# Kernel optimization log

Hardware: AMD Instinct MI355X
Metric: run time of the kernel (lower is better)

## Reference

```python
import jax, jax.numpy as jnp
import numpy as np

N_NODES = 100000
N_EDGES = 3200000
NUM_FEATURES = 128


def gcn_conv(x, edge_index, W, b):
    """PyG-style GCNConv: symmetric normalization with self-loops.
    x: [N, F_in], edge_index: [2, E] (row=src, col=dst), W: [F_in, F_out], b: [F_out].
    """
    n = x.shape[0]
    h = x @ W  # [N, F_out]
    # add self loops
    loop = jnp.arange(n, dtype=edge_index.dtype)
    row = jnp.concatenate([edge_index[0], loop])  # src
    col = jnp.concatenate([edge_index[1], loop])  # dst
    # degree of destination nodes (with self loops), edge weight = 1
    ones = jnp.ones(row.shape[0], dtype=h.dtype)
    deg = jax.ops.segment_sum(ones, col, num_segments=n)  # [N]
    dinv = jnp.where(deg > 0, jax.lax.rsqrt(deg), 0.0)
    norm = dinv[row] * dinv[col]  # [E+N]
    msg = h[row] * norm[:, None]  # gather + scale, [E+N, F_out]
    out = jax.ops.segment_sum(msg, col, num_segments=n)  # scatter-add
    return out + b


def setup_inputs() -> dict:
    key = jax.random.key(0)
    k1, k2, k3, k4 = jax.random.split(key, 4)
    x = jax.random.normal(k1, (N_NODES, NUM_FEATURES), dtype=jnp.float32)
    edge_index = jax.random.randint(k2, (2, N_EDGES), 0, N_NODES, dtype=jnp.int64)
    W1 = jax.random.normal(k3, (NUM_FEATURES, 16), dtype=jnp.float32) * (1.0 / np.sqrt(NUM_FEATURES))
    b1 = jnp.zeros((16,), dtype=jnp.float32)
    W2 = jax.random.normal(k4, (16, 2), dtype=jnp.float32) * (1.0 / np.sqrt(16.0))
    b2 = jnp.zeros((2,), dtype=jnp.float32)
    return {"x": x, "edge_index": edge_index, "W1": W1, "b1": b1, "W2": W2, "b2": b2}


def reference(x, edge_index, W1, b1, W2, b2):
    h = gcn_conv(x, edge_index, W1, b1)
    h = jax.nn.relu(h)
    out = gcn_conv(h, edge_index, W2, b2)
    return out
```

## Files before the change

### kernel.cpp

```cpp
#include <hip/hip_runtime.h>

#define N_FEAT 128
#define F1 16
#define F2 2
#define XPAD 132
#define NPB 512
#define NPB_SHIFT 9
#define BMAX 256
#define CHUNK 8192

typedef int   ev_i4 __attribute__((ext_vector_type(4)));
typedef float ev_f4 __attribute__((ext_vector_type(4)));

__device__ __forceinline__ int4 nt_load_i4(const void* p) {
    ev_i4 v = __builtin_nontemporal_load((const ev_i4*)p);
    return make_int4(v.x, v.y, v.z, v.w);
}
__device__ __forceinline__ int nt_load_i(const int* p) {
    return __builtin_nontemporal_load(p);
}
__device__ __forceinline__ float4 nt_load_f4(const void* p) {
    ev_f4 v = __builtin_nontemporal_load((const ev_f4*)p);
    return make_float4(v.x, v.y, v.z, v.w);
}

__global__ __launch_bounds__(256) void bin_kernel(const int* __restrict__ rowi,
        const int* __restrict__ coli, int* __restrict__ gcur,
        int* __restrict__ ebin, int E, int cap) {
    __shared__ int stage[CHUNK];
    __shared__ unsigned char sbkt[CHUNK];
    __shared__ int cnt[BMAX];
    __shared__ int pos[BMAX];
    __shared__ int runb[BMAX];
    int t = threadIdx.x;
    int base = blockIdx.x * CHUNK;
    int nval = E - base; if (nval > CHUNK) nval = CHUNK;
    cnt[t] = 0;
    __syncthreads();

    int cbuf[32];
#pragma unroll
    for (int j = 0; j < 8; ++j) {
        int idx = base + ((j << 8) + t) * 4;
        if (idx + 3 < E) {
            int4 c4 = nt_load_i4(coli + idx);
            cbuf[j * 4 + 0] = c4.x; cbuf[j * 4 + 1] = c4.y;
            cbuf[j * 4 + 2] = c4.z; cbuf[j * 4 + 3] = c4.w;
        } else {
#pragma unroll
            for (int u = 0; u < 4; ++u) {
                int i2 = idx + u;
                cbuf[j * 4 + u] = (i2 < E) ? coli[i2] : -1;
            }
        }
    }
#pragma unroll
    for (int k = 0; k < 32; ++k)
        if (cbuf[k] >= 0) atomicAdd(&cnt[cbuf[k] >> NPB_SHIFT], 1);
    __syncthreads();

    pos[t] = cnt[t];
    __syncthreads();
    for (int off = 1; off < BMAX; off <<= 1) {
        int a = (t >= off) ? pos[t - off] : 0;
        __syncthreads();
        pos[t] += a;
        __syncthreads();
    }
    int myc = cnt[t];
    int excl = pos[t] - myc;
    if (myc > 0) {
        int g = atomicAdd(&gcur[t], myc);
        runb[t] = t * cap + g - excl;
    }
    __syncthreads();
    cnt[t] = excl;
    __syncthreads();

#pragma unroll
    for (int j = 0; j < 8; ++j) {
        int idx = base + ((j << 8) + t) * 4;
        int rr[4];
        if (idx + 3 < E) {
            int4 r4 = nt_load_i4(rowi + idx);
            rr[0] = r4.x; rr[1] = r4.y; rr[2] = r4.z; rr[3] = r4.w;
        } else {
#pragma unroll
            for (int u = 0; u < 4; ++u) {
                int i2 = idx + u;
                rr[u] = (i2 < E) ? rowi[i2] : 0;
            }
        }
#pragma unroll
        for (int u = 0; u < 4; ++u) {
            int c = cbuf[j * 4 + u];
            if (c >= 0) {
                int b = c >> NPB_SHIFT;
                int lp = atomicAdd(&cnt[b], 1);
                stage[lp] = (rr[u] << NPB_SHIFT) | (c & (NPB - 1));
                sbkt[lp] = (unsigned char)b;
            }
        }
    }
    __syncthreads();
    for (int i = t; i < nval; i += 256)
        ebin[runb[sbkt[i]] + i] = stage[i];
}

__global__ __launch_bounds__(1024) void csr_kernel(const int* __restrict__ gcur,
        const int* __restrict__ ebin, int* __restrict__ rstart, int* __restrict__ degA,
        float* __restrict__ dinv, int* __restrict__ csr, int N, int cap) {
    __shared__ int cnt[NPB];
    __shared__ int sd[NPB];
    int b = blockIdx.x, t = threadIdx.x;
    if (t < NPB) cnt[t] = 0;
    __syncthreads();
    int s = b * cap;
    int e = s + gcur[b];
    for (int i = s + t; i < e; i += 4096) {
        int w[4];
#pragma unroll
        for (int u = 0; u < 4; ++u) {
            int idx = i + u * 1024;
            w[u] = (idx < e) ? nt_load_i(&ebin[idx]) : -1;
        }
#pragma unroll
        for (int u = 0; u < 4; ++u)
            if (w[u] >= 0) atomicAdd(&cnt[w[u] & (NPB - 1)], 1);
    }
    __syncthreads();
    int d = (t < NPB) ? cnt[t] : 0;
    if (t < NPB) sd[t] = d;
    __syncthreads();
    for (int off = 1; off < NPB; off <<= 1) {
        int a = (t < NPB && t >= off) ? sd[t - off] : 0;
        __syncthreads();
        if (t < NPB) sd[t] += a;
        __syncthreads();
    }
    int rs = s + ((t < NPB) ? (sd[t] - d) : 0);
    if (t < NPB) {
        int g = (b << NPB_SHIFT) + t;
        if (g < N) {
            rstart[g] = rs;
            degA[g] = d;
            dinv[g] = rsqrtf((float)(d + 1));
        }
        cnt[t] = rs;
    }
    __syncthreads();
    for (int i = s + t; i < e; i += 4096) {
        int w[4];
#pragma unroll
        for (int u = 0; u < 4; ++u) {
            int idx = i + u * 1024;
            w[u] = (idx < e) ? nt_load_i(&ebin[idx]) : -1;
        }
#pragma unroll
        for (int u = 0; u < 4; ++u) {
            if (w[u] >= 0) {
                int p = atomicAdd(&cnt[w[u] & (NPB - 1)], 1);
                csr[p] = w[u] >> NPB_SHIFT;
            }
        }
    }
}

__global__ __launch_bounds__(256) void gemm1_kernel(
    const float* __restrict__ x, const float* __restrict__ W1,
    const float* __restrict__ dinv, float* __restrict__ hs, int N) {
    __shared__ __align__(16) float wsT[F1][XPAD];
    __shared__ __align__(16) float xs[16][XPAD];
    int t = threadIdx.x;
    for (int i = t; i < N_FEAT * F1; i += 256) {
        int k = i >> 4, f = i & 15;
        wsT[f][k] = W1[i];
    }
    int row0 = blockIdx.x * 16;
    for (int i = t; i < 16 * (N_FEAT / 4); i += 256) {
        int r = i >> 5, k4 = i & 31;
        int row = row0 + r;
        float4 v = (row < N) ? nt_load_f4(x + (size_t)row * N_FEAT + k4 * 4)
                             : make_float4(0.f, 0.f, 0.f, 0.f);
        *(float4*)&xs[r][k4 * 4] = v;
    }
    __syncthreads();
    int rr = t >> 4, f = t & 15;
    int row = row0 + rr;
    if (row >= N) return;
    float acc = 0.f;
#pragma unroll
    for (int k4 = 0; k4 < 32; ++k4) {
        float4 xv = *(const float4*)&xs[rr][k4 * 4];
        float4 wv = *(const float4*)&wsT[f][k4 * 4];
        acc += xv.x * wv.x + xv.y * wv.y + xv.z * wv.z + xv.w * wv.w;
    }
    hs[(size_t)row * F1 + f] = acc * dinv[row];
}

__global__ __launch_bounds__(256) void agg1_kernel(const int* __restrict__ rstart,
        const int* __restrict__ degA, const int* __restrict__ csr,
        const float* __restrict__ hs, const float* __restrict__ dinv,
        const float* __restrict__ b1, const float* __restrict__ W2,
        float* __restrict__ hs2, int N) {
    int t = threadIdx.x;
    int g = blockIdx.x * 16 + (t >> 4);
    int f = t & 15;
    if (g >= N) return;
    int s = rstart[g], e = s + degA[g];
    float acc = hs[(size_t)g * F1 + f];
    int k = s;
    for (; k + 4 <= e; k += 4) {
        int s0 = nt_load_i(&csr[k]);
        int s1 = nt_load_i(&csr[k + 1]);
        int s2 = nt_load_i(&csr[k + 2]);
        int s3 = nt_load_i(&csr[k + 3]);
        float v0 = hs[(size_t)s0 * F1 + f];
        float v1 = hs[(size_t)s1 * F1 + f];
        float v2 = hs[(size_t)s2 * F1 + f];
        float v3 = hs[(size_t)s3 * F1 + f];
        acc += (v0 + v1) + (v2 + v3);
    }
    for (; k < e; ++k) acc += hs[(size_t)nt_load_i(&csr[k]) * F1 + f];
    float di = dinv[g];
    float o = fmaxf(di * acc + b1[f], 0.f);
    float h0 = o * W2[f * F2 + 0];
    float h1 = o * W2[f * F2 + 1];
#pragma unroll
    for (int off = 1; off < 16; off <<= 1) {
        h0 += __shfl_xor(h0, off);
        h1 += __shfl_xor(h1, off);
    }
    if (f == 0) *(float2*)&hs2[(size_t)g * 2] = make_float2(di * h0, di * h1);
}

__global__ __launch_bounds__(256) void agg2_kernel(const int* __restrict__ rstart,
        const int* __restrict__ degA, const int* __restrict__ csr,
        const float* __restrict__ hs2, const float* __restrict__ dinv,
        const float* __restrict__ b2, float* __restrict__ out, int N) {
    int t = threadIdx.x;
    int g = blockIdx.x * 64 + (t >> 2);
    int l = t & 3;
    if (g >= N) return;
    int j = l & 1, c = l >> 1;
    int s = rstart[g], e = s + degA[g];
    float acc = 0.f;
    int k = s + c;
    for (; k + 6 < e; k += 8) {
        int s0 = nt_load_i(&csr[k]);
        int s1 = nt_load_i(&csr[k + 2]);
        int s2 = nt_load_i(&csr[k + 4]);
        int s3 = nt_load_i(&csr[k + 6]);
        acc += hs2[(size_t)s0 * 2 + j] + hs2[(size_t)s1 * 2 + j]
             + hs2[(size_t)s2 * 2 + j] + hs2[(size_t)s3 * 2 + j];
    }
    for (; k < e; k += 2) acc += hs2[(size_t)nt_load_i(&csr[k]) * 2 + j];
    acc += __shfl_xor(acc, 2);
    if (l < 2)
        out[(size_t)g * 2 + j] = dinv[g] * (acc + hs2[(size_t)g * 2 + j]) + b2[j];
}

extern "C" void kernel_launch(void* const* d_in, const int* in_sizes, int n_in,
                              void* d_out, int out_size, void* d_ws, size_t ws_size,
                              hipStream_t stream) {
    const float* x  = (const float*)d_in[0];
    const int*   ei = (const int*)d_in[1];
    const float* W1 = (const float*)d_in[2];
    const float* b1 = (const float*)d_in[3];
    const float* W2 = (const float*)d_in[4];
    const float* b2 = (const float*)d_in[5];
    int N = in_sizes[0] / N_FEAT;
    int E = in_sizes[1] / 2;
    const int* rowi = ei;
    const int* coli = ei + E;
    float* out = (float*)d_out;

    int nbuck = (N + NPB - 1) >> NPB_SHIFT;
    int cap = E / nbuck + 4096;

    size_t NP = ((size_t)N + 1023) & ~(size_t)1023;
    size_t CAPE = ((size_t)nbuck * cap + 1023) & ~(size_t)1023;
    int*   wsI    = (int*)d_ws;
    float* dinv   = (float*)wsI;
    int*   rstart = wsI + NP;
    int*   degA   = wsI + 2 * NP;
    int*   gcur   = wsI + 3 * NP;
    float* hs     = (float*)(wsI + 3 * NP + 512);
    float* hs2    = hs + 16 * NP;
    int*   ebin   = (int*)(hs2 + 2 * NP);
    int*   csr    = ebin + CAPE;

    hipMemsetAsync(gcur, 0, BMAX * sizeof(int), stream);

    bin_kernel<<<(E + CHUNK - 1) / CHUNK, 256, 0, stream>>>(rowi, coli, gcur, ebin, E, cap);
    csr_kernel<<<nbuck, 1024, 0, stream>>>(gcur, ebin, rstart, degA, dinv, csr, N, cap);
    gemm1_kernel<<<(N + 15) / 16, 256, 0, stream>>>(x, W1, dinv, hs, N);
    agg1_kernel<<<(N + 15) / 16, 256, 0, stream>>>(rstart, degA, csr, hs, dinv, b1, W2, hs2, N);
    agg2_kernel<<<(N + 63) / 64, 256, 0, stream>>>(rstart, degA, csr, hs2, dinv, b2, out, N);
}
```

Measured before the change: 258.1 us.

## Fuse first-layer GEMM into CSR kernel and gather fp16 features in aggregation

The separate gemm1 kernel is folded into the CSR-building kernel, so each bucket block computes the scaled x@W1 rows for its 512 nodes, reusing the in-shared dinv values. That block also writes an fp16 copy of the scaled features. agg1 now gathers neighbour rows as half2 from that copy, with 8 lanes per node instead of 16, which halves gather bytes. The risks are reduced precision in neighbour sums and only ~196 large blocks doing the GEMM, which limits parallelism for that phase.

```diff
diff --git a/kernel.cpp b/kernel.cpp
--- a/kernel.cpp
+++ b/kernel.cpp
@@ -1,4 +1,5 @@
 #include <hip/hip_runtime.h>
+#include <hip/hip_fp16.h>
 
 #define N_FEAT 128
 #define F1 16
@@ -107,13 +108,21 @@
         ebin[runb[sbkt[i]] + i] = stage[i];
 }
 
-__global__ __launch_bounds__(1024) void csr_kernel(const int* __restrict__ gcur,
+__global__ __launch_bounds__(1024) void csrg_kernel(const int* __restrict__ gcur,
         const int* __restrict__ ebin, int* __restrict__ rstart, int* __restrict__ degA,
-        float* __restrict__ dinv, int* __restrict__ csr, int N, int cap) {
+        float* __restrict__ dinv, int* __restrict__ csr,
+        const float* __restrict__ x, const float* __restrict__ W1,
+        float* __restrict__ hs, __half* __restrict__ hsH, int N, int cap) {
     __shared__ int cnt[NPB];
     __shared__ int sd[NPB];
+    __shared__ __align__(16) float wsT[F1][XPAD];
+    __shared__ __align__(16) float xs[4][16][XPAD];
     int b = blockIdx.x, t = threadIdx.x;
     if (t < NPB) cnt[t] = 0;
+    for (int i = t; i < N_FEAT * F1; i += 1024) {
+        int k = i >> 4, f = i & 15;
+        wsT[f][k] = W1[i];
+    }
     __syncthreads();
     int s = b * cap;
     int e = s + gcur[b];
@@ -139,13 +148,16 @@
         __syncthreads();
     }
     int rs = s + ((t < NPB) ? (sd[t] - d) : 0);
+    float myinv = rsqrtf((float)(d + 1));
+    __syncthreads();
     if (t < NPB) {
         int g = (b << NPB_SHIFT) + t;
         if (g < N) {
             rstart[g] = rs;
             degA[g] = d;
-            dinv[g] = rsqrtf((float)(d + 1));
-        }
+            dinv[g] = myinv;
+        }
+        ((float*)sd)[t] = myinv;
         cnt[t] = rs;
     }
     __syncthreads();
@@ -164,74 +176,79 @@
             }
         }
     }
-}
-
-__global__ __launch_bounds__(256) void gemm1_kernel(
-    const float* __restrict__ x, const float* __restrict__ W1,
-    const float* __restrict__ dinv, float* __restrict__ hs, int N) {
-    __shared__ __align__(16) float wsT[F1][XPAD];
-    __shared__ __align__(16) float xs[16][XPAD];
-    int t = threadIdx.x;
-    for (int i = t; i < N_FEAT * F1; i += 256) {
-        int k = i >> 4, f = i & 15;
-        wsT[f][k] = W1[i];
-    }
-    int row0 = blockIdx.x * 16;
-    for (int i = t; i < 16 * (N_FEAT / 4); i += 256) {
-        int r = i >> 5, k4 = i & 31;
-        int row = row0 + r;
-        float4 v = (row < N) ? nt_load_f4(x + (size_t)row * N_FEAT + k4 * 4)
-                             : make_float4(0.f, 0.f, 0.f, 0.f);
-        *(float4*)&xs[r][k4 * 4] = v;
-    }
-    __syncthreads();
-    int rr = t >> 4, f = t & 15;
-    int row = row0 + rr;
-    if (row >= N) return;
-    float acc = 0.f;
-#pragma unroll
-    for (int k4 = 0; k4 < 32; ++k4) {
-        float4 xv = *(const float4*)&xs[rr][k4 * 4];
-        float4 wv = *(const float4*)&wsT[f][k4 * 4];
-        acc += xv.x * wv.x + xv.y * wv.y + xv.z * wv.z + xv.w * wv.w;
-    }
-    hs[(size_t)row * F1 + f] = acc * dinv[row];
+    int q = t >> 8;
+    int tq = t & 255;
+    const float* dv = (const float*)sd;
+    for (int it = 0; it < 8; ++it) {
+        int tile = it * 4 + q;
+        int row0 = (b << NPB_SHIFT) + tile * 16;
+        __syncthreads();
+        for (int i = tq; i < 16 * (N_FEAT / 4); i += 256) {
+            int r = i >> 5, k4 = i & 31;
+            int row = row0 + r;
+            float4 v = (row < N) ? nt_load_f4(x + (size_t)row * N_FEAT + k4 * 4)
+                                 : make_float4(0.f, 0.f, 0.f, 0.f);
+            *(float4*)&xs[q][r][k4 * 4] = v;
+        }
+        __syncthreads();
+        int rr = tq >> 4, f = tq & 15;
+        int row = row0 + rr;
+        if (row < N) {
+            float acc = 0.f;
+#pragma unroll
+            for (int k4 = 0; k4 < 32; ++k4) {
+                float4 xv = *(const float4*)&xs[q][rr][k4 * 4];
+                float4 wv = *(const float4*)&wsT[f][k4 * 4];
+                acc += xv.x * wv.x + xv.y * wv.y + xv.z * wv.z + xv.w * wv.w;
+            }
+            float v = acc * dv[tile * 16 + rr];
+            hs[(size_t)row * F1 + f] = v;
+            hsH[(size_t)row * F1 + f] = __float2half(v);
+        }
+    }
 }
 
 __global__ __launch_bounds__(256) void agg1_kernel(const int* __restrict__ rstart,
         const int* __restrict__ degA, const int* __restrict__ csr,
-        const float* __restrict__ hs, const float* __restrict__ dinv,
-        const float* __restrict__ b1, const float* __restrict__ W2,
-        float* __restrict__ hs2, int N) {
+        const float* __restrict__ hs, const __half* __restrict__ hsH,
+        const float* __restrict__ dinv, const float* __restrict__ b1,
+        const float* __restrict__ W2, float* __restrict__ hs2, int N) {
     int t = threadIdx.x;
-    int g = blockIdx.x * 16 + (t >> 4);
-    int f = t & 15;
+    int g = blockIdx.x * 32 + (t >> 3);
+    int q = t & 7;
     if (g >= N) return;
     int s = rstart[g], e = s + degA[g];
-    float acc = hs[(size_t)g * F1 + f];
+    const __half2* h2 = (const __half2*)hsH;
+    float2 acc = *(const float2*)&hs[(size_t)g * F1 + q * 2];
     int k = s;
     for (; k + 4 <= e; k += 4) {
         int s0 = nt_load_i(&csr[k]);
         int s1 = nt_load_i(&csr[k + 1]);
         int s2 = nt_load_i(&csr[k + 2]);
         int s3 = nt_load_i(&csr[k + 3]);
-        float v0 = hs[(size_t)s0 * F1 + f];
-        float v1 = hs[(size_t)s1 * F1 + f];
-        float v2 = hs[(size_t)s2 * F1 + f];
-        float v3 = hs[(size_t)s3 * F1 + f];
-        acc += (v0 + v1) + (v2 + v3);
-    }
-    for (; k < e; ++k) acc += hs[(size_t)nt_load_i(&csr[k]) * F1 + f];
+        float2 v0 = __half22float2(h2[(size_t)s0 * 8 + q]);
+        float2 v1 = __half22float2(h2[(size_t)s1 * 8 + q]);
+        float2 v2 = __half22float2(h2[(size_t)s2 * 8 + q]);
+        float2 v3 = __half22float2(h2[(size_t)s3 * 8 + q]);
+        acc.x += (v0.x + v1.x) + (v2.x + v3.x);
+        acc.y += (v0.y + v1.y) + (v2.y + v3.y);
+    }
+    for (; k < e; ++k) {
+        float2 v = __half22float2(h2[(size_t)nt_load_i(&csr[k]) * 8 + q]);
+        acc.x += v.x; acc.y += v.y;
+    }
     float di = dinv[g];
-    float o = fmaxf(di * acc + b1[f], 0.f);
-    float h0 = o * W2[f * F2 + 0];
-    float h1 = o * W2[f * F2 + 1];
-#pragma unroll
-    for (int off = 1; off < 16; off <<= 1) {
+    int f0 = q * 2;
+    float o0 = fmaxf(di * acc.x + b1[f0 + 0], 0.f);
+    float o1 = fmaxf(di * acc.y + b1[f0 + 1], 0.f);
+    float h0 = o0 * W2[(f0 + 0) * F2 + 0] + o1 * W2[(f0 + 1) * F2 + 0];
+    float h1 = o0 * W2[(f0 + 0) * F2 + 1] + o1 * W2[(f0 + 1) * F2 + 1];
+#pragma unroll
+    for (int off = 1; off < 8; off <<= 1) {
         h0 += __shfl_xor(h0, off);
         h1 += __shfl_xor(h1, off);
     }
-    if (f == 0) *(float2*)&hs2[(size_t)g * 2] = make_float2(di * h0, di * h1);
+    if (q == 0) *(float2*)&hs2[(size_t)g * 2] = make_float2(di * h0, di * h1);
 }
 
 __global__ __launch_bounds__(256) void agg2_kernel(const int* __restrict__ rstart,
@@ -286,15 +303,17 @@
     int*   degA   = wsI + 2 * NP;
     int*   gcur   = wsI + 3 * NP;
     float* hs     = (float*)(wsI + 3 * NP + 512);
-    float* hs2    = hs + 16 * NP;
+    __half* hsH   = (__half*)(hs + 16 * NP);
+    float* hs2    = (float*)((int*)hsH + 8 * NP);
     int*   ebin   = (int*)(hs2 + 2 * NP);
     int*   csr    = ebin + CAPE;
 
     hipMemsetAsync(gcur, 0, BMAX * sizeof(int), stream);
 
     bin_kernel<<<(E + CHUNK - 1) / CHUNK, 256, 0, stream>>>(rowi, coli, gcur, ebin, E, cap);
-    csr_kernel<<<nbuck, 1024, 0, stream>>>(gcur, ebin, rstart, degA, dinv, csr, N, cap);
-    gemm1_kernel<<<(N + 15) / 16, 256, 0, stream>>>(x, W1, dinv, hs, N);
-    agg1_kernel<<<(N + 15) / 16, 256, 0, stream>>>(rstart, degA, csr, hs, dinv, b1, W2, hs2, N);
+    csrg_kernel<<<nbuck, 1024, 0, stream>>>(gcur, ebin, rstart, degA, dinv, csr,
+                                            x, W1, hs, hsH, N, cap);
+    agg1_kernel<<<(N + 31) / 32, 256, 0, stream>>>(rstart, degA, csr, hs, hsH,
+                                                   dinv, b1, W2, hs2, N);
     agg2_kernel<<<(N + 63) / 64, 256, 0, stream>>>(rstart, degA, csr, hs2, dinv, b2, out, N);
 }
```

After: 252.8 us. 1.02x faster.
